# Kernel tuning notes

Measured on AMD Instinct MI355X. Metric: run time of the kernel, lower is better.

## Reference

```python
import jax, jax.numpy as jnp
import numpy as np

H_MODEL = 1024
N_HEADS = 16
N_KV_HEADS = 4
HEAD_DIM = 64
SLIDING_WINDOW = 512
B, S = 2, 2048
NEG_INF = -1e9


def rotate_half(x):
    half = x.shape[-1] // 2
    return jnp.concatenate([-x[..., half:], x[..., :half]], axis=-1)


def setup_inputs() -> dict:
    key = jax.random.key(0)
    ks = jax.random.split(key, 8)
    hidden_states = jax.random.normal(ks[0], (B, S, H_MODEL), dtype=jnp.float32)
    # RoPE tables (HF style): cos/sin of shape [1, S, head_dim]
    inv_freq = 1.0 / (10000.0 ** (jnp.arange(0, HEAD_DIM, 2, dtype=jnp.float32) / HEAD_DIM))
    pos = jnp.arange(S, dtype=jnp.float32)
    freqs = jnp.einsum('s,d->sd', pos, inv_freq)            # [S, D/2]
    emb = jnp.concatenate([freqs, freqs], axis=-1)          # [S, D]
    cos = jnp.cos(emb)[None]                                # [1, S, D]
    sin = jnp.sin(emb)[None]
    # additive causal + sliding-window mask [1,1,S,S]
    i = jnp.arange(S)[:, None]
    j = jnp.arange(S)[None, :]
    allowed = (j <= i) & (i - j < SLIDING_WINDOW)
    attention_mask = jnp.where(allowed, 0.0, NEG_INF).astype(jnp.float32)[None, None]
    # projection weights (torch Linear stores [out, in]; y = x @ W.T)
    std = 0.02
    Wq = jax.random.normal(ks[1], (N_HEADS * HEAD_DIM, H_MODEL), dtype=jnp.float32) * std
    Wk = jax.random.normal(ks[2], (N_KV_HEADS * HEAD_DIM, H_MODEL), dtype=jnp.float32) * std
    Wv = jax.random.normal(ks[3], (N_KV_HEADS * HEAD_DIM, H_MODEL), dtype=jnp.float32) * std
    Wo = jax.random.normal(ks[4], (H_MODEL, N_HEADS * HEAD_DIM), dtype=jnp.float32) * std
    return {"hidden_states": hidden_states, "cos": cos, "sin": sin,
            "attention_mask": attention_mask, "Wq": Wq, "Wk": Wk, "Wv": Wv, "Wo": Wo}


def reference(hidden_states, cos, sin, attention_mask, Wq, Wk, Wv, Wo):
    b, s, _ = hidden_states.shape
    G = N_HEADS // N_KV_HEADS
    scaling = HEAD_DIM ** -0.5
    # QKV projections -> [B, H, S, D]
    q = jnp.einsum('bsh,oh->bso', hidden_states, Wq).reshape(b, s, N_HEADS, HEAD_DIM).transpose(0, 2, 1, 3)
    k = jnp.einsum('bsh,oh->bso', hidden_states, Wk).reshape(b, s, N_KV_HEADS, HEAD_DIM).transpose(0, 2, 1, 3)
    v = jnp.einsum('bsh,oh->bso', hidden_states, Wv).reshape(b, s, N_KV_HEADS, HEAD_DIM).transpose(0, 2, 1, 3)
    # RoPE (cos/sin broadcast over head dim via unsqueeze(1))
    c = cos[:, None, :, :]
    sn = sin[:, None, :, :]
    q = q * c + rotate_half(q) * sn
    k = k * c + rotate_half(k) * sn
    # GQA eager attention: group query heads over kv heads
    qg = q.reshape(b, N_KV_HEADS, G, s, HEAD_DIM)
    scores = jnp.einsum('bkgqd,bkpd->bkgqp', qg, k) * scaling  # [B,Hkv,G,S,S]
    scores = scores + attention_mask[:, :, None, :, :]
    probs = jax.nn.softmax(scores.astype(jnp.float32), axis=-1).astype(q.dtype)
    out = jnp.einsum('bkgqp,bkpd->bkgqd', probs, v)            # [B,Hkv,G,S,D]
    out = out.reshape(b, N_HEADS, s, HEAD_DIM).transpose(0, 2, 1, 3).reshape(b, s, N_HEADS * HEAD_DIM)
    return jnp.einsum('bso,ho->bsh', out, Wo)
```

## Files before the change

### kernel.cpp

```cpp
#include <hip/hip_runtime.h>
#include <hip/hip_bf16.h>

#define S_LEN 2048
#define NH 16
#define NKV 4
#define HD 64
#define WIN 512
#define BATCH 2

typedef __bf16 bf16_8 __attribute__((ext_vector_type(8)));
typedef float f32x4 __attribute__((ext_vector_type(4)));

__device__ inline bf16_8 cvt8(f32x4 a, f32x4 b) {
    bf16_8 r;
    r[0] = (__bf16)a[0]; r[1] = (__bf16)a[1]; r[2] = (__bf16)a[2]; r[3] = (__bf16)a[3];
    r[4] = (__bf16)b[0]; r[5] = (__bf16)b[1]; r[6] = (__bf16)b[2]; r[7] = (__bf16)b[3];
    return r;
}

__global__ __launch_bounds__(256) void cvt_pack(
    const float* __restrict__ hs, const float* __restrict__ Wq,
    const float* __restrict__ Wk, const float* __restrict__ Wv,
    const float* __restrict__ Wo,
    __bf16* __restrict__ hsb, __bf16* __restrict__ Wqp,
    __bf16* __restrict__ Wkp, __bf16* __restrict__ Wvp,
    __bf16* __restrict__ Wop)
{
    int i = blockIdx.x * 256 + threadIdx.x;
    if (i < 524288) {
        const size_t j = (size_t)i * 8;
        const f32x4 a = *(const f32x4*)(hs + j);
        const f32x4 b = *(const f32x4*)(hs + j + 4);
        *(bf16_8*)(hsb + j) = cvt8(a, b);
        return;
    }
    i -= 524288;
    const float* S; __bf16* P;
    if (i < 131072)      { S = Wq; P = Wqp; }
    else if (i < 163840) { S = Wk; P = Wkp; i -= 131072; }
    else if (i < 196608) { S = Wv; P = Wvp; i -= 163840; }
    else                 { S = Wo; P = Wop; i -= 196608; }
    const int n = i >> 7;
    const int k = (i & 127) << 3;
    const f32x4 a = *(const f32x4*)(S + (size_t)n * 1024 + k);
    const f32x4 b = *(const f32x4*)(S + (size_t)n * 1024 + k + 4);
    const size_t dst = ((size_t)((n >> 4) * 32 + (k >> 5)) << 9)
                     + ((size_t)((n & 15) | (((k >> 3) & 3) << 4)) << 3);
    *(bf16_8*)(P + dst) = cvt8(a, b);
}

__device__ __forceinline__ void gemm64x128(
    const __bf16* __restrict__ Ap, const __bf16* __restrict__ Bq,
    int row0, __bf16* __restrict__ As, int tid, f32x4 acc[2][4])
{
    const int wave = tid >> 6;
    const int lane = tid & 63;
    const int wm   = wave & 1;
    const int ar = tid >> 2, ac = (tid & 3) << 4;
    const int fm = lane & 15;
    const int fj = (lane >> 4) << 3;
    const f32x4 fzero = {0.f, 0.f, 0.f, 0.f};
#pragma unroll
    for (int i = 0; i < 2; ++i)
#pragma unroll
        for (int nt = 0; nt < 4; ++nt) acc[i][nt] = fzero;

    const size_t aoff = (size_t)(row0 + ar) * 1024 + ac;
    bf16_8 b0[4], b1[4];
    {
        const bf16_8 a0 = *(const bf16_8*)&Ap[aoff];
        const bf16_8 a1 = *(const bf16_8*)&Ap[aoff + 8];
        *(bf16_8*)&As[ar * 72 + ac]     = a0;
        *(bf16_8*)&As[ar * 72 + ac + 8] = a1;
#pragma unroll
        for (int nt = 0; nt < 4; ++nt)
            b0[nt] = *(const bf16_8*)(Bq + nt * 16384);
    }
    __syncthreads();

    for (int it = 0; it < 16; ++it) {
        const int cur = it & 1;
        const bool pf = it < 15;
        bf16_8 qa0, qa1, bn[4];
        if (pf) {
            qa0 = *(const bf16_8*)&Ap[aoff + (it + 1) * 64];
            qa1 = *(const bf16_8*)&Ap[aoff + (it + 1) * 64 + 8];
        }
#pragma unroll
        for (int nt = 0; nt < 4; ++nt)
            b1[nt] = *(const bf16_8*)(Bq + nt * 16384 + (it * 2 + 1) * 512);

        bf16_8 af0[2];
#pragma unroll
        for (int i = 0; i < 2; ++i)
            af0[i] = *(const bf16_8*)&As[cur * 4608 + (wm * 32 + i * 16 + fm) * 72 + fj];
#pragma unroll
        for (int i = 0; i < 2; ++i)
#pragma unroll
            for (int nt = 0; nt < 4; ++nt)
                acc[i][nt] = __builtin_amdgcn_mfma_f32_16x16x32_bf16(af0[i], b0[nt], acc[i][nt], 0, 0, 0);

        if (pf) {
#pragma unroll
            for (int nt = 0; nt < 4; ++nt)
                bn[nt] = *(const bf16_8*)(Bq + nt * 16384 + (it + 1) * 1024);
        }
        bf16_8 af1[2];
#pragma unroll
        for (int i = 0; i < 2; ++i)
            af1[i] = *(const bf16_8*)&As[cur * 4608 + (wm * 32 + i * 16 + fm) * 72 + 32 + fj];
#pragma unroll
        for (int i = 0; i < 2; ++i)
#pragma unroll
            for (int nt = 0; nt < 4; ++nt)
                acc[i][nt] = __builtin_amdgcn_mfma_f32_16x16x32_bf16(af1[i], b1[nt], acc[i][nt], 0, 0, 0);

        if (pf) {
            const int nb = cur ^ 1;
            *(bf16_8*)&As[nb * 4608 + ar * 72 + ac]     = qa0;
            *(bf16_8*)&As[nb * 4608 + ar * 72 + ac + 8] = qa1;
#pragma unroll
            for (int nt = 0; nt < 4; ++nt) b0[nt] = bn[nt];
        }
        __syncthreads();
    }
}

__global__ __launch_bounds__(256) void gemm_qkv(
    const __bf16* __restrict__ A,
    const __bf16* __restrict__ Wqp,
    const __bf16* __restrict__ Wkp,
    const __bf16* __restrict__ Wvp,
    __bf16* __restrict__ Qb,
    __bf16* __restrict__ Kf,
    __bf16* __restrict__ Vf,
    const float* __restrict__ cosb,
    const float* __restrict__ sinb)
{
    __shared__ __align__(16) __bf16 smem[9216];

    const int tid  = threadIdx.x;
    const int wave = tid >> 6;
    const int lane = tid & 63;
    const int wm   = wave & 1;
    const int wn   = wave >> 1;
    const int fm   = lane & 15;

    const int row0 = blockIdx.x * 64;
    const int by   = blockIdx.y;

    const __bf16* Bp; int colb; int mode;
    if (by < 8)       { Bp = Wqp; colb = by * 128;        mode = 0; }
    else if (by < 10) { Bp = Wkp; colb = (by - 8) * 128;  mode = 1; }
    else              { Bp = Wvp; colb = (by - 10) * 128; mode = 2; }
    const int col0 = colb;

    const __bf16* Bq = Bp + (size_t)((colb + wn * 64) >> 4) * 16384 + (lane << 3);
    f32x4 acc[2][4];
    gemm64x128(A, Bq, row0, smem, tid, acc);

    const int drow = (lane >> 4) << 2;
    const int cq   = col0 + wn * 64;
    const int bb   = row0 >> 11;
    const int sk0  = row0 & (S_LEN - 1);

    if (mode == 0) {
#pragma unroll
        for (int i = 0; i < 2; ++i) {
#pragma unroll
            for (int r = 0; r < 4; ++r) {
                const int row = row0 + wm * 32 + i * 16 + drow + r;
                const int s   = row & (S_LEN - 1);
#pragma unroll
                for (int nt = 0; nt < 2; ++nt) {
                    const int d = nt * 16 + fm;
                    const float c1 = cosb[s * HD + d];
                    const float s1 = sinb[s * HD + d];
                    const float c2 = cosb[s * HD + d + 32];
                    const float s2 = sinb[s * HD + d + 32];
                    const float x1 = acc[i][nt][r];
                    const float x2 = acc[i][nt + 2][r];
                    Qb[(size_t)row * 1024 + cq + d]      = (__bf16)(x1 * c1 - x2 * s1);
                    Qb[(size_t)row * 1024 + cq + d + 32] = (__bf16)(x2 * c2 + x1 * s2);
                }
            }
        }
    } else if (mode == 1) {
        __bf16* T = smem;
#pragma unroll
        for (int i = 0; i < 2; ++i) {
#pragma unroll
            for (int r = 0; r < 4; ++r) {
                const int kl = wm * 32 + i * 16 + drow + r;
                const int s  = sk0 + kl;
#pragma unroll
                for (int nt = 0; nt < 2; ++nt) {
                    const int d = nt * 16 + fm;
                    const float c1 = cosb[s * HD + d];
                    const float s1 = sinb[s * HD + d];
                    const float c2 = cosb[s * HD + d + 32];
                    const float s2 = sinb[s * HD + d + 32];
                    const float x1 = acc[i][nt][r];
                    const float x2 = acc[i][nt + 2][r];
                    T[kl * 136 + wn * 64 + d]      = (__bf16)(x1 * c1 - x2 * s1);
                    T[kl * 136 + wn * 64 + d + 32] = (__bf16)(x2 * c2 + x1 * s2);
                }
            }
        }
        __syncthreads();
#pragma unroll
        for (int c = 0; c < 4; ++c) {
            const int tile = c * 4 + wave;
            const int hh  = tile >> 3;
            const int kt4 = (tile >> 1) & 3;
            const int dd  = tile & 1;
            const int key = kt4 * 16 + fm;
            const int dl  = dd * 32 + ((lane >> 4) << 3);
            const bf16_8 v = *(const bf16_8*)&T[key * 136 + hh * 64 + dl];
            const int khg = (col0 + hh * 64) >> 6;
            const int ktg = (sk0 >> 4) + kt4;
            *(bf16_8*)&Kf[(size_t)(bb * NKV + khg) * 131072 + (size_t)(ktg * 2 + dd) * 512 + lane * 8] = v;
        }
    } else {
        __bf16* T2 = smem;
#pragma unroll
        for (int i = 0; i < 2; ++i)
#pragma unroll
            for (int r = 0; r < 4; ++r)
#pragma unroll
                for (int nt = 0; nt < 4; ++nt)
                    T2[(wn * 64 + nt * 16 + fm) * 72 + wm * 32 + i * 16 + drow + r] =
                        (__bf16)acc[i][nt][r];
        __syncthreads();
#pragma unroll
        for (int c = 0; c < 4; ++c) {
            const int tile = c * 4 + wave;
            const int hh  = tile >> 3;
            const int dd4 = (tile >> 1) & 3;
            const int ks  = tile & 1;
            const int dl  = dd4 * 16 + fm;
            const int key = ks * 32 + ((lane >> 4) << 3);
            const bf16_8 v = *(const bf16_8*)&T2[(hh * 64 + dl) * 72 + key];
            const int khg = (col0 + hh * 64) >> 6;
            const int kvg = (sk0 >> 5) + ks;
            *(bf16_8*)&Vf[(size_t)(bb * NKV + khg) * 131072 + (size_t)(dd4 * 64 + kvg) * 512 + lane * 8] = v;
        }
    }
}

__global__ __launch_bounds__(256) void gemm_o(
    const __bf16* __restrict__ A,
    const __bf16* __restrict__ Bp,
    float* __restrict__ C)
{
    __shared__ __align__(16) __bf16 smem[9216];

    const int tid  = threadIdx.x;
    const int wave = tid >> 6;
    const int lane = tid & 63;
    const int wm   = wave & 1;
    const int wn   = wave >> 1;

    const int row0 = blockIdx.x * 64;
    const int colb = blockIdx.y * 128;

    const __bf16* Bq = Bp + (size_t)((colb + wn * 64) >> 4) * 16384 + (lane << 3);
    f32x4 acc[2][4];
    gemm64x128(A, Bq, row0, smem, tid, acc);

    const int fm = lane & 15;
    const int drow = (lane >> 4) << 2;
#pragma unroll
    for (int i = 0; i < 2; ++i)
#pragma unroll
        for (int r = 0; r < 4; ++r) {
            const int row = row0 + wm * 32 + i * 16 + drow + r;
#pragma unroll
            for (int nt = 0; nt < 4; ++nt)
                C[(size_t)row * 1024 + colb + wn * 64 + nt * 16 + fm] = acc[i][nt][r];
        }
}

__global__ __launch_bounds__(256) void attn_pk(const __bf16* __restrict__ Q,
                                               const __bf16* __restrict__ Kf,
                                               const __bf16* __restrict__ Vf,
                                               __bf16* __restrict__ O)
{
    __shared__ __align__(16) __bf16 Ps[4][16][72];

    const int tid  = threadIdx.x;
    const int wave = tid >> 6;
    const int lane = tid & 63;

    const int qt = blockIdx.x & (S_LEN / 64 - 1);
    const int h  = (blockIdx.x >> 5) & (NH - 1);
    const int b  = blockIdx.x >> 9;
    const int kh = h >> 2;

    const int q0 = qt * 64;
    const int qw = q0 + wave * 16;

    const int fm = lane & 15;
    const int fj = (lane >> 4) << 3;

    const size_t qrow = (size_t)(b * S_LEN + qw + fm) * (NH * HD) + h * HD;
    const bf16_8 qf0 = *(const bf16_8*)&Q[qrow + fj];
    const bf16_8 qf1 = *(const bf16_8*)&Q[qrow + 32 + fj];

    const __bf16* Kfb = Kf + (size_t)(b * NKV + kh) * 131072 + lane * 8;
    const __bf16* Vfb = Vf + (size_t)(b * NKV + kh) * 131072 + lane * 8;

    const f32x4 fzero = {0.f, 0.f, 0.f, 0.f};
    f32x4 oacc[4];
    float l[4];
#pragma unroll
    for (int nt = 0; nt < 4; ++nt) oacc[nt] = fzero;
#pragma unroll
    for (int r = 0; r < 4; ++r) l[r] = 0.f;

    const int qbase = qw + ((lane >> 4) << 2);

    const int lo  = (qw >= WIN) ? ((qw - WIN + 1) & ~63) : 0;
    const int hi  = (qw + 15) & ~63;
    const int nit = ((hi - lo) >> 6) + 1;

    for (int it = 0; it < nit; ++it) {
        const int kb = lo + (it << 6);

        f32x4 sc[4];
        const int ktb = kb >> 4;
#pragma unroll
        for (int t4 = 0; t4 < 4; ++t4) {
            const bf16_8 k0 = *(const bf16_8*)(Kfb + (size_t)((ktb + t4) * 2) * 512);
            const bf16_8 k1 = *(const bf16_8*)(Kfb + (size_t)((ktb + t4) * 2 + 1) * 512);
            f32x4 s = fzero;
            s = __builtin_amdgcn_mfma_f32_16x16x32_bf16(qf0, k0, s, 0, 0, 0);
            s = __builtin_amdgcn_mfma_f32_16x16x32_bf16(qf1, k1, s, 0, 0, 0);
            sc[t4] = s;
        }

#pragma unroll
        for (int t4 = 0; t4 < 4; ++t4) {
            const int ki = kb + t4 * 16 + fm;
#pragma unroll
            for (int r = 0; r < 4; ++r) {
                const int qr = qbase + r;
                const float e = __expf(sc[t4][r] * 0.125f);
                const float p = (ki <= qr && qr - ki < WIN) ? e : 0.f;
                l[r] += p;
                Ps[wave][((lane >> 4) << 2) + r][t4 * 16 + fm] = (__bf16)p;
            }
        }

        const bf16_8 pf0 = *(const bf16_8*)&Ps[wave][fm][fj];
        const bf16_8 pf1 = *(const bf16_8*)&Ps[wave][fm][32 + fj];

        const int kvb = kb >> 5;
#pragma unroll
        for (int nt = 0; nt < 4; ++nt) {
            const bf16_8 v0 = *(const bf16_8*)(Vfb + (size_t)(nt * 64 + kvb) * 512);
            const bf16_8 v1 = *(const bf16_8*)(Vfb + (size_t)(nt * 64 + kvb + 1) * 512);
            oacc[nt] = __builtin_amdgcn_mfma_f32_16x16x32_bf16(pf0, v0, oacc[nt], 0, 0, 0);
            oacc[nt] = __builtin_amdgcn_mfma_f32_16x16x32_bf16(pf1, v1, oacc[nt], 0, 0, 0);
        }
    }

#pragma unroll
    for (int off = 8; off > 0; off >>= 1)
#pragma unroll
        for (int r = 0; r < 4; ++r)
            l[r] += __shfl_xor(l[r], off, 64);

    const int drow = (lane >> 4) << 2;
    float inv[4];
#pragma unroll
    for (int r = 0; r < 4; ++r) inv[r] = 1.0f / l[r];
#pragma unroll
    for (int nt = 0; nt < 4; ++nt)
#pragma unroll
        for (int r = 0; r < 4; ++r) {
            const size_t off = (size_t)(b * S_LEN + qw + drow + r) * (NH * HD) + h * HD + nt * 16 + fm;
            O[off] = (__bf16)(oacc[nt][r] * inv[r]);
        }
}

extern "C" void kernel_launch(void* const* d_in, const int* in_sizes, int n_in,
                              void* d_out, int out_size, void* d_ws, size_t ws_size,
                              hipStream_t stream)
{
    const float* hs   = (const float*)d_in[0];
    const float* cosb = (const float*)d_in[1];
    const float* sinb = (const float*)d_in[2];
    const float* Wq = (const float*)d_in[4];
    const float* Wk = (const float*)d_in[5];
    const float* Wv = (const float*)d_in[6];
    const float* Wo = (const float*)d_in[7];

    const int M = BATCH * S_LEN;

    __bf16* hsb = (__bf16*)d_ws;
    __bf16* Wqp = hsb + (size_t)M * 1024;
    __bf16* Wkp = Wqp + 1024 * 1024;
    __bf16* Wvp = Wkp + 256 * 1024;
    __bf16* Wop = Wvp + 256 * 1024;
    __bf16* Qb  = Wop + 1024 * 1024;
    __bf16* Kfb = Qb  + (size_t)M * 1024;
    __bf16* Vfb = Kfb + (size_t)8 * 131072;
    __bf16* Ob  = Vfb + (size_t)8 * 131072;

    dim3 blk(256);
    cvt_pack<<<3328, blk, 0, stream>>>(hs, Wq, Wk, Wv, Wo,
                                       hsb, Wqp, Wkp, Wvp, Wop);

    gemm_qkv<<<dim3(64, 12), blk, 0, stream>>>(hsb, Wqp, Wkp, Wvp,
                                               Qb, Kfb, Vfb, cosb, sinb);

    attn_pk<<<BATCH * NH * (S_LEN / 64), blk, 0, stream>>>(Qb, Kfb, Vfb, Ob);

    gemm_o<<<dim3(64, 8), blk, 0, stream>>>(Ob, Wop, (float*)d_out);
}
```

Baseline: 159.7 us.

## Use direct global-to-LDS loads with XOR swizzle in GEMM and remap attention blocks

The shared GEMM helper now stages the A tile with global_load_lds (direct global-to-LDS DMA) into an unpadded, XOR-swizzled 64-wide layout. This replaces the register round-trip and the padded 72-stride layout. Both B fragment halves are now prefetched one iteration ahead, and the loop is unrolled by two. Separately, the attention kernel permutes block indices so that consecutive hardware block IDs land on different XCDs while blocks sharing K/V stay grouped, aiming at better L2 locality. Risks include correctness of the swizzle versus the DMA write pattern, and higher register pressure from the extra B prefetch.

```diff
diff --git a/kernel.cpp b/kernel.cpp
--- a/kernel.cpp
+++ b/kernel.cpp
@@ -16,6 +16,12 @@
     r[0] = (__bf16)a[0]; r[1] = (__bf16)a[1]; r[2] = (__bf16)a[2]; r[3] = (__bf16)a[3];
     r[4] = (__bf16)b[0]; r[5] = (__bf16)b[1]; r[6] = (__bf16)b[2]; r[7] = (__bf16)b[3];
     return r;
+}
+
+typedef __attribute__((address_space(1))) const unsigned int guint;
+typedef __attribute__((address_space(3))) unsigned int luint;
+__device__ __forceinline__ void gload16(const void* g, void* l) {
+    __builtin_amdgcn_global_load_lds((guint*)g, (luint*)l, 16, 0, 0);
 }
 
 __global__ __launch_bounds__(256) void cvt_pack(
@@ -56,59 +62,62 @@
     const int wave = tid >> 6;
     const int lane = tid & 63;
     const int wm   = wave & 1;
-    const int ar = tid >> 2, ac = (tid & 3) << 4;
-    const int fm = lane & 15;
-    const int fj = (lane >> 4) << 3;
+    const int fm   = lane & 15;
+    const int fj   = (lane >> 4) << 3;
     const f32x4 fzero = {0.f, 0.f, 0.f, 0.f};
 #pragma unroll
     for (int i = 0; i < 2; ++i)
 #pragma unroll
         for (int nt = 0; nt < 4; ++nt) acc[i][nt] = fzero;
 
-    const size_t aoff = (size_t)(row0 + ar) * 1024 + ac;
+    const int srow = (wave << 4) + (lane >> 3);
+    const int xr   = (((lane & 7) << 3)) ^ ((srow & 7) << 3);
+    const __bf16* gA = Ap + (size_t)(row0 + srow) * 1024 + xr;
+    __bf16* dstB0 = As + wave * 1024;
+
+    const int r0  = wm * 32 + fm;
+    const int xk0 = fj ^ ((fm & 7) << 3);
+    const int xk1 = xk0 ^ 32;
+
+    gload16(gA, dstB0);
+    gload16(gA + 8192, dstB0 + 512);
     bf16_8 b0[4], b1[4];
-    {
-        const bf16_8 a0 = *(const bf16_8*)&Ap[aoff];
-        const bf16_8 a1 = *(const bf16_8*)&Ap[aoff + 8];
-        *(bf16_8*)&As[ar * 72 + ac]     = a0;
-        *(bf16_8*)&As[ar * 72 + ac + 8] = a1;
-#pragma unroll
-        for (int nt = 0; nt < 4; ++nt)
-            b0[nt] = *(const bf16_8*)(Bq + nt * 16384);
+#pragma unroll
+    for (int nt = 0; nt < 4; ++nt) {
+        b0[nt] = *(const bf16_8*)(Bq + nt * 16384);
+        b1[nt] = *(const bf16_8*)(Bq + nt * 16384 + 512);
     }
     __syncthreads();
 
+#pragma unroll 2
     for (int it = 0; it < 16; ++it) {
         const int cur = it & 1;
         const bool pf = it < 15;
-        bf16_8 qa0, qa1, bn[4];
+        bf16_8 nb0[4], nb1[4];
         if (pf) {
-            qa0 = *(const bf16_8*)&Ap[aoff + (it + 1) * 64];
-            qa1 = *(const bf16_8*)&Ap[aoff + (it + 1) * 64 + 8];
-        }
-#pragma unroll
-        for (int nt = 0; nt < 4; ++nt)
-            b1[nt] = *(const bf16_8*)(Bq + nt * 16384 + (it * 2 + 1) * 512);
-
+            __bf16* dst = As + (cur ^ 1) * 4096 + wave * 1024;
+            gload16(gA + (it + 1) * 64, dst);
+            gload16(gA + (it + 1) * 64 + 8192, dst + 512);
+#pragma unroll
+            for (int nt = 0; nt < 4; ++nt) {
+                nb0[nt] = *(const bf16_8*)(Bq + nt * 16384 + (it + 1) * 1024);
+                nb1[nt] = *(const bf16_8*)(Bq + nt * 16384 + (it + 1) * 1024 + 512);
+            }
+        }
+
+        const __bf16* Ab = As + cur * 4096;
         bf16_8 af0[2];
-#pragma unroll
-        for (int i = 0; i < 2; ++i)
-            af0[i] = *(const bf16_8*)&As[cur * 4608 + (wm * 32 + i * 16 + fm) * 72 + fj];
+        af0[0] = *(const bf16_8*)&Ab[r0 * 64 + xk0];
+        af0[1] = *(const bf16_8*)&Ab[(r0 + 16) * 64 + xk0];
 #pragma unroll
         for (int i = 0; i < 2; ++i)
 #pragma unroll
             for (int nt = 0; nt < 4; ++nt)
                 acc[i][nt] = __builtin_amdgcn_mfma_f32_16x16x32_bf16(af0[i], b0[nt], acc[i][nt], 0, 0, 0);
 
-        if (pf) {
-#pragma unroll
-            for (int nt = 0; nt < 4; ++nt)
-                bn[nt] = *(const bf16_8*)(Bq + nt * 16384 + (it + 1) * 1024);
-        }
         bf16_8 af1[2];
-#pragma unroll
-        for (int i = 0; i < 2; ++i)
-            af1[i] = *(const bf16_8*)&As[cur * 4608 + (wm * 32 + i * 16 + fm) * 72 + 32 + fj];
+        af1[0] = *(const bf16_8*)&Ab[r0 * 64 + xk1];
+        af1[1] = *(const bf16_8*)&Ab[(r0 + 16) * 64 + xk1];
 #pragma unroll
         for (int i = 0; i < 2; ++i)
 #pragma unroll
@@ -116,11 +125,8 @@
                 acc[i][nt] = __builtin_amdgcn_mfma_f32_16x16x32_bf16(af1[i], b1[nt], acc[i][nt], 0, 0, 0);
 
         if (pf) {
-            const int nb = cur ^ 1;
-            *(bf16_8*)&As[nb * 4608 + ar * 72 + ac]     = qa0;
-            *(bf16_8*)&As[nb * 4608 + ar * 72 + ac + 8] = qa1;
-#pragma unroll
-            for (int nt = 0; nt < 4; ++nt) b0[nt] = bn[nt];
+#pragma unroll
+            for (int nt = 0; nt < 4; ++nt) { b0[nt] = nb0[nt]; b1[nt] = nb1[nt]; }
         }
         __syncthreads();
     }
@@ -292,9 +298,12 @@
     const int wave = tid >> 6;
     const int lane = tid & 63;
 
-    const int qt = blockIdx.x & (S_LEN / 64 - 1);
-    const int h  = (blockIdx.x >> 5) & (NH - 1);
-    const int b  = blockIdx.x >> 9;
+    const int bid0 = blockIdx.x;
+    const int bid  = (bid0 & 7) * 128 + (bid0 >> 3);
+
+    const int qt = bid & (S_LEN / 64 - 1);
+    const int h  = (bid >> 5) & (NH - 1);
+    const int b  = bid >> 9;
     const int kh = h >> 2;
 
     const int q0 = qt * 64;
```

Result: no change. 162.5 us (+1.7%).
